# Kernel optimization log

Measured on AMD Instinct MI355X. Metric: run time of the kernel, lower is better.

The kernel has to match this reference:

```python
import jax, jax.numpy as jnp
import numpy as np

# (a1,a2,a3,a4,b1,b2,b3,b4,xi_E,xi_I,mu,e,k) per oscillator type
PARAMS = {
    1: (0.0, 5.0, 5.0, 1.0, 0.0, -1.0, 1.0, 0.0, 0.0, 0.0, 5.0, 0.001, 500),
    2: (0.5, 0.55, 0.55, -0.5, 0.5, -0.55, -0.55, -0.5, 0.0, 0.0, 1.0, 0.001, 50),
    3: (0.5, 0.6, 0.55, 0.5, -0.5, -0.6, -0.55, 0.5, 0.0, 0.0, 1.0, 0.001, 50),
    4: (-0.5, 0.55, 0.55, -0.5, -0.5, -0.55, -0.55, 0.5, 0.0, 0.0, 1.0, 0.001, 50),
    5: (-0.9, 0.9, 0.9, -0.9, 0.9, -0.9, -0.9, 0.9, 0.0, 0.0, 1.0, 0.001, 50),
    6: (-0.9, 0.9, 0.9, -0.9, 0.9, -0.9, -0.9, 0.9, 0.0, 0.0, 1.0, 0.001, 300),
    7: (-5.0, 5.0, 5.0, -5.0, 1.0, -1.0, -1.0, 1.0, 0.0, 0.0, 1.0, 0.001, 50),
    8: (-5.0, 5.0, 5.0, -5.0, 1.0, -1.0, -1.0, 1.0, 0.0, 0.0, 1.0, 0.001, 300),
}
N_STEPS = 100  # torch runs t = 0..99 producing LORS[1..100], then max over those


def _lee_forward(x, osc_type):
    a1, a2, a3, a4, b1, b2, b3, b4, xi_E, xi_I, mu, e, k = PARAMS[osc_type]
    # stimulus with tiny sign-dependent offset; constant over time
    sim0 = x + e * jnp.sign(x)
    damp = jnp.exp(-k * sim0 * sim0)   # exp(-k*sim0^2), constant over time
    omega = jnp.tanh(mu * sim0)        # Omega[t+1] is the same every step
    E0 = jnp.full_like(x, 0.2)
    I0 = jnp.zeros_like(x)
    L0 = jnp.full_like(x, 0.2)
    m0 = jnp.full_like(x, -jnp.inf)    # running max over LORS[1..100]

    def step(carry, _):
        E, I, L, m = carry
        E1 = jnp.tanh(mu * (a1 * L + a2 * E - a3 * I + a4 * sim0 - xi_E))
        I1 = jnp.tanh(mu * (b1 * L - b2 * E - b3 * I + b4 * sim0 - xi_I))
        L1 = (E1 - I1) * damp + omega
        return (E1, I1, L1, jnp.maximum(m, L1)), None

    (_, _, _, m), _ = jax.lax.scan(step, (E0, I0, L0, m0), None, length=N_STEPS)
    return m


def setup_inputs() -> dict:
    key = jax.random.key(0)
    x = jax.random.normal(key, (2048, 512), dtype=jnp.float32)
    return {"x": x, "oscillator_type": 1}


def reference(x, oscillator_type):
    # output shape == x.shape: time-max-pooled LORS activation
    return _lee_forward(x, oscillator_type)
```

## Files before the change

kernel.cpp:

```cpp
#include <hip/hip_runtime.h>
#include <math.h>


#define N_STEPS 100

typedef float v2f __attribute__((ext_vector_type(2)));
__device__ __forceinline__ v2f splat2(float s){ v2f v; v.x = s; v.y = s; return v; }

__constant__ float PAR[8][13] = {
    { 0.0f,  5.0f,  5.0f,  1.0f,  0.0f, -1.0f,  1.0f,  0.0f, 0.0f, 0.0f, 5.0f, 0.001f, 500.0f},
    { 0.5f,  0.55f, 0.55f, -0.5f,  0.5f, -0.55f, -0.55f, -0.5f, 0.0f, 0.0f, 1.0f, 0.001f, 50.0f},
    { 0.5f,  0.6f,  0.55f,  0.5f, -0.5f, -0.6f,  -0.55f,  0.5f, 0.0f, 0.0f, 1.0f, 0.001f, 50.0f},
    {-0.5f,  0.55f, 0.55f, -0.5f, -0.5f, -0.55f, -0.55f,  0.5f, 0.0f, 0.0f, 1.0f, 0.001f, 50.0f},
    {-0.9f,  0.9f,  0.9f,  -0.9f,  0.9f, -0.9f,  -0.9f,   0.9f, 0.0f, 0.0f, 1.0f, 0.001f, 50.0f},
    {-0.9f,  0.9f,  0.9f,  -0.9f,  0.9f, -0.9f,  -0.9f,   0.9f, 0.0f, 0.0f, 1.0f, 0.001f, 300.0f},
    {-5.0f,  5.0f,  5.0f,  -5.0f,  1.0f, -1.0f,  -1.0f,   1.0f, 0.0f, 0.0f, 1.0f, 0.001f, 50.0f},
    {-5.0f,  5.0f,  5.0f,  -5.0f,  1.0f, -1.0f,  -1.0f,   1.0f, 0.0f, 0.0f, 1.0f, 0.001f, 300.0f},
};

__device__ __forceinline__ float xla_tanhf(float x) {
#pragma clang fp contract(off)
    float ax = fabsf(x);
    float xc = fminf(fmaxf(x, -7.99881172180175781f), 7.99881172180175781f);
    float x2 = xc * xc;
    float p = -2.76076847742355e-16f;
    p = fmaf(p, x2, 2.00018790482477e-13f);
    p = fmaf(p, x2, -8.60467152213735e-11f);
    p = fmaf(p, x2, 5.12229709037114e-08f);
    p = fmaf(p, x2, 1.48572235717979e-05f);
    p = fmaf(p, x2, 6.37261928875436e-04f);
    p = fmaf(p, x2, 4.89352455891786e-03f);
    float num = xc * p;
    float q = 1.19825839466702e-06f;
    q = fmaf(q, x2, 1.18534705686654e-04f);
    q = fmaf(q, x2, 2.26843463243900e-03f);
    q = fmaf(q, x2, 4.89352518554385e-03f);
    float r = num / q;
    return (ax < 0.0004f) ? x : r;
}

__device__ __forceinline__ float div_exact(float a, float b) {
#pragma clang fp contract(off)
    float r = __builtin_amdgcn_rcpf(b);
    float e = fmaf(-b, r, 1.0f);
    r = fmaf(e, r, r);
    float e2 = fmaf(-b, r, 1.0f);
    r = fmaf(e2, r, r);
    float y = a * r;
    float rem = fmaf(-b, y, a);
    y = fmaf(rem, r, y);
    float rem2 = fmaf(-b, y, a);
    y = fmaf(rem2, r, y);
    return y;
}

__device__ __forceinline__ v2f xla_tanh2(v2f x) {
#pragma clang fp contract(off)
    const float C = 7.99881172180175781f;
    v2f xc = __builtin_elementwise_min(__builtin_elementwise_max(x, splat2(-C)), splat2(C));
    v2f x2 = xc * xc;
    v2f p = splat2(-2.76076847742355e-16f);
    p = __builtin_elementwise_fma(p, x2, splat2(2.00018790482477e-13f));
    p = __builtin_elementwise_fma(p, x2, splat2(-8.60467152213735e-11f));
    p = __builtin_elementwise_fma(p, x2, splat2(5.12229709037114e-08f));
    p = __builtin_elementwise_fma(p, x2, splat2(1.48572235717979e-05f));
    p = __builtin_elementwise_fma(p, x2, splat2(6.37261928875436e-04f));
    p = __builtin_elementwise_fma(p, x2, splat2(4.89352455891786e-03f));
    v2f num = xc * p;
    v2f q = splat2(1.19825839466702e-06f);
    q = __builtin_elementwise_fma(q, x2, splat2(1.18534705686654e-04f));
    q = __builtin_elementwise_fma(q, x2, splat2(2.26843463243900e-03f));
    q = __builtin_elementwise_fma(q, x2, splat2(4.89352518554385e-03f));
    float rE = div_exact(num.x, q.x);
    float rI = div_exact(num.y, q.y);
    v2f r;
    r.x = (fabsf(x.x) < 0.0004f) ? x.x : rE;
    r.y = (fabsf(x.y) < 0.0004f) ? x.y : rI;
    return r;
}

__device__ __forceinline__ float xla_expf(float x) {
#pragma clang fp contract(off)
    float xc = fminf(fmaxf(x, -88.3762626647949f), 88.3762626647950f);
    float fx = floorf(fmaf(xc, 1.44269504088896341f, 0.5f));
    float r = fmaf(fx, -0.693359375f, xc);
    r = fmaf(fx, 2.12194440e-4f, r);
    float r2 = r * r;
    float y = 1.9875691500e-4f;
    y = fmaf(y, r, 1.3981999507e-3f);
    y = fmaf(y, r, 8.3334519073e-3f);
    y = fmaf(y, r, 4.1665795894e-2f);
    y = fmaf(y, r, 1.6666665459e-1f);
    y = fmaf(y, r, 5.0000001201e-1f);
    y = fmaf(y, r2, r);
    y = y + 1.0f;
    int n2 = (int)fx;
    float p2n = __int_as_float((n2 + 127) << 23);
    return y * p2n;
}

__device__ __forceinline__ void preamble(float xv, const float* p,
                                         float& sim0, float& damp, float& omega) {
#pragma clang fp contract(off)
    float mu = p[10], e = p[11], k = p[12];
    float sgn  = (xv > 0.0f) ? 1.0f : ((xv < 0.0f) ? -1.0f : 0.0f);
    sim0 = fmaf(e, sgn, xv);
    float targ = (-k * sim0) * sim0;
    damp  = xla_expf(targ);
    omega = xla_tanhf(mu * sim0);
}

__device__ __forceinline__ bool fast_omega(float damp, float omega) {
    return (2.0f * damp) < (fabsf(omega) * 0x1p-26f);
}

__device__ __forceinline__ bool slow_t1(float xv, float e) {
#pragma clang fp contract(off)
    float sgn  = (xv > 0.0f) ? 1.0f : ((xv < 0.0f) ? -1.0f : 0.0f);
    float sim0 = fmaf(e, sgn, xv);
    return fabsf(sim0) <= 0.21f;
}

__device__ __forceinline__ float loop_t1(float sim0, float damp, float omega) {
#pragma clang fp contract(off)
    float E = 0.2f, I = 0.0f;
    float Dmax = -INFINITY;
    for (int s = 0; s < N_STEPS; ++s) {
        float tE = 5.0f * E;
        v2f mulc; mulc.x = -5.0f; mulc.y = -1.0f;
        v2f iv   = splat2(I);
        v2f addv; addv.x = tE;    addv.y = E;
        v2f u = __builtin_elementwise_fma(mulc, iv, addv);
        float sE = u.x + sim0;
        v2f pre; pre.x = sE; pre.y = u.y;
        v2f args = splat2(5.0f) * pre;
        v2f t = xla_tanh2(args);
        float D = t.x - t.y;
        Dmax = fmaxf(Dmax, D);
        E = t.x; I = t.y;
    }
    return fmaf(Dmax, damp, omega);
}

__device__ __forceinline__ float loop_gen(const float* p, float sim0,
                                          float damp, float omega) {
#pragma clang fp contract(off)
    float a1 = p[0], a2 = p[1], a3 = p[2], a4 = p[3];
    float b1 = p[4], b2 = p[5], b3 = p[6], b4 = p[7];
    float xiE = p[8], xiI = p[9], mu = p[10];
    float nb2 = -b2;
    float E = 0.2f, I = 0.0f, L = 0.2f;
    float m = -INFINITY;
    for (int s = 0; s < N_STEPS; ++s) {
        float tE = a2 * E;
        float uE = fmaf(a1, L, tE);
        uE = fmaf(-a3, I, uE);
        uE = fmaf(a4, sim0, uE);
        uE = uE - xiE;
        float argE = mu * uE;
        float tI = nb2 * E;
        float uI = fmaf(b1, L, tI);
        uI = fmaf(-b3, I, uI);
        uI = fmaf(b4, sim0, uI);
        uI = uI - xiI;
        float argI = mu * uI;
        float E1 = xla_tanhf(argE);
        float I1 = xla_tanhf(argI);
        float d = E1 - I1;
        L = fmaf(d, damp, omega);
        E = E1; I = I1;
        m = fmaxf(m, L);
    }
    return m;
}

__device__ __forceinline__ bool classify_slow(float xv, int t, const float* p) {
    if (t == 1) return slow_t1(xv, p[11]);
    float sim0, damp, omega;
    preamble(xv, p, sim0, damp, omega);
    return !fast_omega(damp, omega);
}


__global__ __launch_bounds__(256)
void k_count(const float* __restrict__ x, const int* __restrict__ osc_type,
             unsigned* __restrict__ bcount, int n)
{
    __shared__ unsigned wc[4];
    int i = blockIdx.x * 256 + threadIdx.x;
    int t = *osc_type;
    const float* p = PAR[t - 1];
    bool slow = (i < n) && classify_slow(x[i], t, p);
    unsigned long long mask = __ballot(slow);
    int lane = threadIdx.x & 63, wid = threadIdx.x >> 6;
    if (lane == 0) wc[wid] = (unsigned)__popcll(mask);
    __syncthreads();
    if (threadIdx.x == 0) bcount[blockIdx.x] = wc[0] + wc[1] + wc[2] + wc[3];
}

__global__ __launch_bounds__(256)
void k_fill(const float* __restrict__ x, const int* __restrict__ osc_type,
            float* __restrict__ out, unsigned* __restrict__ bcount,
            unsigned* __restrict__ wl, int n, int NB)
{
#pragma clang fp contract(off)
    __shared__ unsigned sums[256];
    __shared__ unsigned woff[4];
    int tid = threadIdx.x;
    int bid = blockIdx.x;

    unsigned s = 0;
    for (int j = tid; j < bid; j += 256) s += bcount[j];
    sums[tid] = s;
    __syncthreads();
    for (int off = 128; off > 0; off >>= 1) {
        if (tid < off) sums[tid] += sums[tid + off];
        __syncthreads();
    }
    unsigned bbase = sums[0];

    int i = bid * 256 + tid;
    bool active = (i < n);
    int t = *osc_type;
    const float* p = PAR[t - 1];
    float xv = active ? x[i] : 1.0e9f;
    bool slow = active && classify_slow(xv, t, p);
    if (active && !slow) {
        float mu = p[10], e = p[11];
        float sgn  = (xv > 0.0f) ? 1.0f : ((xv < 0.0f) ? -1.0f : 0.0f);
        float sim0 = fmaf(e, sgn, xv);
        out[i] = xla_tanhf(mu * sim0);
    }
    unsigned long long mask = __ballot(slow);
    int lane = tid & 63, wid = tid >> 6;
    if (lane == 0) woff[wid] = (unsigned)__popcll(mask);
    __syncthreads();
    if (slow) {
        unsigned base = bbase;
        for (int w = 0; w < wid; ++w) base += woff[w];
        base += (unsigned)__popcll(mask & ((1ull << lane) - 1ull));
        wl[base] = (unsigned)i;
    }
    if (tid == 0 && bid == NB - 1)
        bcount[NB] = bbase + woff[0] + woff[1] + woff[2] + woff[3];
}

__global__ __launch_bounds__(64)
void k_process(const float* __restrict__ x, const int* __restrict__ osc_type,
               float* __restrict__ out, const unsigned* __restrict__ total_p,
               const unsigned* __restrict__ wl)
{
#pragma clang fp contract(off)
    unsigned total = *total_p;
    int t = *osc_type;
    const float* p = PAR[t - 1];
    unsigned stride = gridDim.x * 64u;
    for (unsigned tid = blockIdx.x * 64u + threadIdx.x; tid < total; tid += stride) {
        int i = (int)wl[tid];
        float sim0, damp, omega;
        preamble(x[i], p, sim0, damp, omega);
        out[i] = (t == 1) ? loop_t1(sim0, damp, omega)
                          : loop_gen(p, sim0, damp, omega);
    }
}

__global__ __launch_bounds__(256)
void k_monolithic(const float* __restrict__ x, const int* __restrict__ osc_type,
                  float* __restrict__ out, int n)
{
#pragma clang fp contract(off)
    int i = blockIdx.x * 256 + threadIdx.x;
    if (i >= n) return;
    int t = *osc_type;
    const float* p = PAR[t - 1];
    float sim0, damp, omega;
    preamble(x[i], p, sim0, damp, omega);
    if (fast_omega(damp, omega)) { out[i] = omega; return; }
    out[i] = (t == 1) ? loop_t1(sim0, damp, omega)
                      : loop_gen(p, sim0, damp, omega);
}

extern "C" void kernel_launch(void* const* d_in, const int* in_sizes, int n_in,
                              void* d_out, int out_size, void* d_ws, size_t ws_size,
                              hipStream_t stream) {
    const float* x        = (const float*)d_in[0];
    const int*   osc_type = (const int*)d_in[1];
    float*       out      = (float*)d_out;
    int n = in_sizes[0];
    int NB = (n + 255) / 256;

    size_t needed = ((size_t)NB + 1 + (size_t)n) * sizeof(unsigned);
    if (ws_size >= needed) {
        unsigned* bcount = (unsigned*)d_ws;
        unsigned* wl     = bcount + NB + 1;
        k_count  <<<NB, 256, 0, stream>>>(x, osc_type, bcount, n);
        k_fill   <<<NB, 256, 0, stream>>>(x, osc_type, out, bcount, wl, n, NB);
        k_process<<<4096, 64, 0, stream>>>(x, osc_type, out, bcount + NB, wl);
    } else {
        k_monolithic<<<NB, 256, 0, stream>>>(x, osc_type, out, n);
    }
}
```

Baseline: 43.33 us.

## Split type-1 slow elements into core and edge worklists with early-exit on periodic orbit

Type-1 elements that need the full recurrence are now split into two classes by |sim0|: a core band that runs the full 100-step loop, and an edge band written to the back of the worklist. The edge band runs a loop that steps twice at a time and exits once every lane in the wave has reached a period-2 fixed point, since further steps cannot change the running max. This removes recurrence work for elements that converge quickly and groups like-converging elements into the same waves so the wave-wide exit can fire. The cost is extra ballots and prefix sums in the count and fill kernels, plus a per-pair check. The early exit assumes a bit-exact period-2 cycle, and the 0.13 band threshold looks tuned to the test data.

```diff
diff --git a/kernel.cpp b/kernel.cpp
--- a/kernel.cpp
+++ b/kernel.cpp
@@ -114,30 +114,51 @@
     return (2.0f * damp) < (fabsf(omega) * 0x1p-26f);
 }
 
-__device__ __forceinline__ bool slow_t1(float xv, float e) {
+__device__ __forceinline__ int classify3_t1(float xv, float e) {
 #pragma clang fp contract(off)
     float sgn  = (xv > 0.0f) ? 1.0f : ((xv < 0.0f) ? -1.0f : 0.0f);
     float sim0 = fmaf(e, sgn, xv);
-    return fabsf(sim0) <= 0.21f;
+    float a = fabsf(sim0);
+    if (a > 0.21f) return 0;
+    if (a > 0.13f) return 2;
+    return 1;
+}
+
+__device__ __forceinline__ void step_t1(float& E, float& I, float& Dmax, float sim0) {
+#pragma clang fp contract(off)
+    float tE = 5.0f * E;
+    v2f mulc; mulc.x = -5.0f; mulc.y = -1.0f;
+    v2f iv   = splat2(I);
+    v2f addv; addv.x = tE;    addv.y = E;
+    v2f u = __builtin_elementwise_fma(mulc, iv, addv);
+    float sE = u.x + sim0;
+    v2f pre; pre.x = sE; pre.y = u.y;
+    v2f args = splat2(5.0f) * pre;
+    v2f t = xla_tanh2(args);
+    float D = t.x - t.y;
+    Dmax = fmaxf(Dmax, D);
+    E = t.x; I = t.y;
 }
 
 __device__ __forceinline__ float loop_t1(float sim0, float damp, float omega) {
 #pragma clang fp contract(off)
     float E = 0.2f, I = 0.0f;
     float Dmax = -INFINITY;
-    for (int s = 0; s < N_STEPS; ++s) {
-        float tE = 5.0f * E;
-        v2f mulc; mulc.x = -5.0f; mulc.y = -1.0f;
-        v2f iv   = splat2(I);
-        v2f addv; addv.x = tE;    addv.y = E;
-        v2f u = __builtin_elementwise_fma(mulc, iv, addv);
-        float sE = u.x + sim0;
-        v2f pre; pre.x = sE; pre.y = u.y;
-        v2f args = splat2(5.0f) * pre;
-        v2f t = xla_tanh2(args);
-        float D = t.x - t.y;
-        Dmax = fmaxf(Dmax, D);
-        E = t.x; I = t.y;
+    for (int s = 0; s < N_STEPS; ++s) step_t1(E, I, Dmax, sim0);
+    return fmaf(Dmax, damp, omega);
+}
+
+__device__ __forceinline__ float loop_t1_edge(float sim0, float damp, float omega) {
+#pragma clang fp contract(off)
+    float E = 0.2f, I = 0.0f;
+    float Dmax = -INFINITY;
+    for (int s = 0; s < N_STEPS; s += 2) {
+        float Em2 = E, Im2 = I;
+        step_t1(E, I, Dmax, sim0);
+        step_t1(E, I, Dmax, sim0);
+        int per = (__float_as_int(E) == __float_as_int(Em2)) &
+                  (__float_as_int(I) == __float_as_int(Im2));
+        if (__all(per)) break;
     }
     return fmaf(Dmax, damp, omega);
 }
@@ -174,93 +195,123 @@
     return m;
 }
 
-__device__ __forceinline__ bool classify_slow(float xv, int t, const float* p) {
-    if (t == 1) return slow_t1(xv, p[11]);
+__device__ __forceinline__ int classify(float xv, int t, const float* p) {
+    if (t == 1) return classify3_t1(xv, p[11]);
     float sim0, damp, omega;
     preamble(xv, p, sim0, damp, omega);
-    return !fast_omega(damp, omega);
+    return fast_omega(damp, omega) ? 0 : 1;
 }
 
 
 __global__ __launch_bounds__(256)
 void k_count(const float* __restrict__ x, const int* __restrict__ osc_type,
-             unsigned* __restrict__ bcount, int n)
+             unsigned* __restrict__ bcntA, unsigned* __restrict__ bcntB, int n)
 {
-    __shared__ unsigned wc[4];
+    __shared__ unsigned wcA[4], wcB[4];
     int i = blockIdx.x * 256 + threadIdx.x;
     int t = *osc_type;
     const float* p = PAR[t - 1];
-    bool slow = (i < n) && classify_slow(x[i], t, p);
-    unsigned long long mask = __ballot(slow);
+    int cls = (i < n) ? classify(x[i], t, p) : 0;
+    unsigned long long mA = __ballot(cls == 1);
+    unsigned long long mB = __ballot(cls == 2);
     int lane = threadIdx.x & 63, wid = threadIdx.x >> 6;
-    if (lane == 0) wc[wid] = (unsigned)__popcll(mask);
+    if (lane == 0) { wcA[wid] = (unsigned)__popcll(mA); wcB[wid] = (unsigned)__popcll(mB); }
     __syncthreads();
-    if (threadIdx.x == 0) bcount[blockIdx.x] = wc[0] + wc[1] + wc[2] + wc[3];
+    if (threadIdx.x == 0) {
+        bcntA[blockIdx.x] = wcA[0] + wcA[1] + wcA[2] + wcA[3];
+        bcntB[blockIdx.x] = wcB[0] + wcB[1] + wcB[2] + wcB[3];
+    }
 }
 
 __global__ __launch_bounds__(256)
 void k_fill(const float* __restrict__ x, const int* __restrict__ osc_type,
-            float* __restrict__ out, unsigned* __restrict__ bcount,
-            unsigned* __restrict__ wl, int n, int NB)
+            float* __restrict__ out, unsigned* __restrict__ bcntA,
+            unsigned* __restrict__ bcntB, unsigned* __restrict__ wl,
+            int n, int NB)
 {
 #pragma clang fp contract(off)
-    __shared__ unsigned sums[256];
-    __shared__ unsigned woff[4];
+    __shared__ unsigned sumsA[256], sumsB[256];
+    __shared__ unsigned woffA[4], woffB[4];
     int tid = threadIdx.x;
     int bid = blockIdx.x;
 
-    unsigned s = 0;
-    for (int j = tid; j < bid; j += 256) s += bcount[j];
-    sums[tid] = s;
+    unsigned sA = 0, sB = 0;
+    for (int j = tid; j < bid; j += 256) { sA += bcntA[j]; sB += bcntB[j]; }
+    sumsA[tid] = sA; sumsB[tid] = sB;
     __syncthreads();
     for (int off = 128; off > 0; off >>= 1) {
-        if (tid < off) sums[tid] += sums[tid + off];
+        if (tid < off) { sumsA[tid] += sumsA[tid + off]; sumsB[tid] += sumsB[tid + off]; }
         __syncthreads();
     }
-    unsigned bbase = sums[0];
+    unsigned baseA = sumsA[0], baseB = sumsB[0];
 
     int i = bid * 256 + tid;
     bool active = (i < n);
     int t = *osc_type;
     const float* p = PAR[t - 1];
     float xv = active ? x[i] : 1.0e9f;
-    bool slow = active && classify_slow(xv, t, p);
-    if (active && !slow) {
+    int cls = active ? classify(xv, t, p) : 0;
+    if (active && cls == 0) {
         float mu = p[10], e = p[11];
         float sgn  = (xv > 0.0f) ? 1.0f : ((xv < 0.0f) ? -1.0f : 0.0f);
         float sim0 = fmaf(e, sgn, xv);
         out[i] = xla_tanhf(mu * sim0);
     }
-    unsigned long long mask = __ballot(slow);
+    unsigned long long mA = __ballot(cls == 1);
+    unsigned long long mB = __ballot(cls == 2);
     int lane = tid & 63, wid = tid >> 6;
-    if (lane == 0) woff[wid] = (unsigned)__popcll(mask);
+    if (lane == 0) { woffA[wid] = (unsigned)__popcll(mA); woffB[wid] = (unsigned)__popcll(mB); }
     __syncthreads();
-    if (slow) {
-        unsigned base = bbase;
-        for (int w = 0; w < wid; ++w) base += woff[w];
-        base += (unsigned)__popcll(mask & ((1ull << lane) - 1ull));
-        wl[base] = (unsigned)i;
-    }
-    if (tid == 0 && bid == NB - 1)
-        bcount[NB] = bbase + woff[0] + woff[1] + woff[2] + woff[3];
+    unsigned long long below = (1ull << lane) - 1ull;
+    if (cls == 1) {
+        unsigned pos = baseA;
+        for (int w = 0; w < wid; ++w) pos += woffA[w];
+        pos += (unsigned)__popcll(mA & below);
+        wl[pos] = (unsigned)i;
+    } else if (cls == 2) {
+        unsigned pos = baseB;
+        for (int w = 0; w < wid; ++w) pos += woffB[w];
+        pos += (unsigned)__popcll(mB & below);
+        wl[(unsigned)n - 1u - pos] = (unsigned)i;
+    }
+    if (tid == 0 && bid == NB - 1) {
+        bcntA[NB] = baseA + woffA[0] + woffA[1] + woffA[2] + woffA[3];
+        bcntB[NB] = baseB + woffB[0] + woffB[1] + woffB[2] + woffB[3];
+    }
 }
 
 __global__ __launch_bounds__(64)
 void k_process(const float* __restrict__ x, const int* __restrict__ osc_type,
-               float* __restrict__ out, const unsigned* __restrict__ total_p,
-               const unsigned* __restrict__ wl)
+               float* __restrict__ out, const unsigned* __restrict__ bcntA,
+               const unsigned* __restrict__ bcntB, const unsigned* __restrict__ wl,
+               int n, int NB)
 {
 #pragma clang fp contract(off)
-    unsigned total = *total_p;
+    unsigned Tc = bcntA[NB];
+    unsigned Te = bcntB[NB];
+    unsigned total = Tc + Te;
     int t = *osc_type;
     const float* p = PAR[t - 1];
     unsigned stride = gridDim.x * 64u;
     for (unsigned tid = blockIdx.x * 64u + threadIdx.x; tid < total; tid += stride) {
-        int i = (int)wl[tid];
-        float sim0, damp, omega;
-        preamble(x[i], p, sim0, damp, omega);
-        out[i] = (t == 1) ? loop_t1(sim0, damp, omega)
-                          : loop_gen(p, sim0, damp, omega);
+        if (t == 1) {
+            if (tid < Tc) {
+                int i = (int)wl[tid];
+                float sim0, damp, omega;
+                preamble(x[i], p, sim0, damp, omega);
+                out[i] = loop_t1(sim0, damp, omega);
+            } else {
+                int i = (int)wl[(unsigned)n - 1u - (tid - Tc)];
+                float sim0, damp, omega;
+                preamble(x[i], p, sim0, damp, omega);
+                out[i] = loop_t1_edge(sim0, damp, omega);
+            }
+        } else {
+            int i = (int)wl[tid];
+            float sim0, damp, omega;
+            preamble(x[i], p, sim0, damp, omega);
+            out[i] = loop_gen(p, sim0, damp, omega);
+        }
     }
 }
 
@@ -289,13 +340,14 @@
     int n = in_sizes[0];
     int NB = (n + 255) / 256;
 
-    size_t needed = ((size_t)NB + 1 + (size_t)n) * sizeof(unsigned);
+    size_t needed = (2 * ((size_t)NB + 1) + (size_t)n) * sizeof(unsigned);
     if (ws_size >= needed) {
-        unsigned* bcount = (unsigned*)d_ws;
-        unsigned* wl     = bcount + NB + 1;
-        k_count  <<<NB, 256, 0, stream>>>(x, osc_type, bcount, n);
-        k_fill   <<<NB, 256, 0, stream>>>(x, osc_type, out, bcount, wl, n, NB);
-        k_process<<<4096, 64, 0, stream>>>(x, osc_type, out, bcount + NB, wl);
+        unsigned* bcntA = (unsigned*)d_ws;
+        unsigned* bcntB = bcntA + NB + 1;
+        unsigned* wl    = bcntB + NB + 1;
+        k_count  <<<NB, 256, 0, stream>>>(x, osc_type, bcntA, bcntB, n);
+        k_fill   <<<NB, 256, 0, stream>>>(x, osc_type, out, bcntA, bcntB, wl, n, NB);
+        k_process<<<4096, 64, 0, stream>>>(x, osc_type, out, bcntA, bcntB, wl, n, NB);
     } else {
         k_monolithic<<<NB, 256, 0, stream>>>(x, osc_type, out, n);
     }
```

After: 49.57 us. 14.4% more time.
